# Kernel optimization log

Hardware: AMD Instinct MI355X
Metric: run time of the kernel (lower is better)

The kernel has to match this reference:

```python
import jax, jax.numpy as jnp
import numpy as np

N, D, H, Y = 2048, 768, 12, 64


def setup_inputs() -> dict:
    key = jax.random.key(0)
    kg, kq, kk = jax.random.split(key, 3)
    g = jax.random.normal(kg, (N, D), dtype=jnp.float32)
    Wq = jax.random.normal(kq, (H, Y, D), dtype=jnp.float32)
    Wk = jax.random.normal(kk, (H, Y, D), dtype=jnp.float32)
    return {"g": g, "Wq": Wq, "Wk": Wk}


def reference(g, Wq, Wk):
    # g: [N, D]; Wq, Wk: [H, Y, D]
    beta = 1.0 / jnp.sqrt(jnp.asarray(Y, dtype=g.dtype))
    K = jnp.einsum('kd,hzd->khz', g, Wk)          # [N, H, Y]
    Q = jnp.einsum('qd,hzd->qhz', g, Wq)          # [N, H, Y]
    scores = beta * jnp.einsum('qhz,khz->hqk', Q, K)  # [H, N, N]
    A = jax.nn.logsumexp(scores, axis=-1)         # [H, N]
    return (-1.0 / beta) * A.sum()
```

## Files before the change

kernel.cpp:

```cpp
#include <hip/hip_runtime.h>
#include <hip/hip_bf16.h>

#define NN 2048
#define DD 768
#define HH 12
#define HW 1536
#define SPLITS 4
#define KPW (NN/SPLITS)
#define NCH (KPW/64)
#define LDP 72

typedef __attribute__((ext_vector_type(8))) short bf16x8;
typedef __attribute__((ext_vector_type(4))) float f32x4;

__device__ __forceinline__ float exp2g(float x) { return __builtin_amdgcn_exp2f(x); }
__device__ __forceinline__ float log2g(float x) { return __builtin_amdgcn_logf(x); }

#define QSCALE 0.18033688011112042f

__device__ __forceinline__ short b16(float x) {
  __hip_bfloat16 h = __float2bfloat16(x);
  return *reinterpret_cast<short*>(&h);
}
__device__ __forceinline__ bf16x8 cvt8(float4 a, float4 b, float sc) {
  bf16x8 r;
  r[0] = b16(a.x * sc); r[1] = b16(a.y * sc);
  r[2] = b16(a.z * sc); r[3] = b16(a.w * sc);
  r[4] = b16(b.x * sc); r[5] = b16(b.y * sc);
  r[6] = b16(b.z * sc); r[7] = b16(b.w * sc);
  return r;
}

__global__ __launch_bounds__(256) void proj_kernel(
    const float* __restrict__ g, const float* __restrict__ Wq,
    const float* __restrict__ Wk, __hip_bfloat16* __restrict__ QK,
    float* __restrict__ out) {
  __shared__ __align__(16) __hip_bfloat16 As[2][64 * LDP];
  __shared__ __align__(16) __hip_bfloat16 Bs[2][64 * LDP];
  const int t = threadIdx.x;
  const int wave = t >> 6, lane = t & 63;
  const int lr = lane & 15, lg = lane >> 4;
  const int wm = wave & 1, wn = wave >> 1;
  const int bm = blockIdx.x, bn = blockIdx.y;
  if (bm == 0 && bn == 0 && t == 0) out[0] = 0.0f;

  const float* Wsrc = (bn < 12) ? (Wq + bn * 64 * DD) : (Wk + (bn - 12) * 64 * DD);
  const float sc = (bn < 12) ? QSCALE : 1.0f;

  const int r0 = t >> 3, s0c = (t & 7) * 8;
  const int r1 = r0 + 32;

  f32x4 acc[2][2] = {};

  {
    const float* ga0 = g + (bm * 64 + r0) * DD + s0c;
    const float* ga1 = g + (bm * 64 + r1) * DD + s0c;
    const float* gb0 = Wsrc + r0 * DD + s0c;
    const float* gb1 = Wsrc + r1 * DD + s0c;
    *reinterpret_cast<bf16x8*>(&As[0][r0 * LDP + s0c]) =
        cvt8(*(const float4*)ga0, *(const float4*)(ga0 + 4), 1.0f);
    *reinterpret_cast<bf16x8*>(&As[0][r1 * LDP + s0c]) =
        cvt8(*(const float4*)ga1, *(const float4*)(ga1 + 4), 1.0f);
    *reinterpret_cast<bf16x8*>(&Bs[0][r0 * LDP + s0c]) =
        cvt8(*(const float4*)gb0, *(const float4*)(gb0 + 4), sc);
    *reinterpret_cast<bf16x8*>(&Bs[0][r1 * LDP + s0c]) =
        cvt8(*(const float4*)gb1, *(const float4*)(gb1 + 4), sc);
  }
  __syncthreads();

  for (int it = 0; it < 12; ++it) {
    const int cur = it & 1;
    float4 pa0, pa1, pa2, pa3, pb0, pb1, pb2, pb3;
    if (it < 11) {
      int kt = (it + 1) * 64;
      const float* ga0 = g + (bm * 64 + r0) * DD + kt + s0c;
      const float* ga1 = g + (bm * 64 + r1) * DD + kt + s0c;
      const float* gb0 = Wsrc + r0 * DD + kt + s0c;
      const float* gb1 = Wsrc + r1 * DD + kt + s0c;
      pa0 = *(const float4*)ga0; pa1 = *(const float4*)(ga0 + 4);
      pa2 = *(const float4*)ga1; pa3 = *(const float4*)(ga1 + 4);
      pb0 = *(const float4*)gb0; pb1 = *(const float4*)(gb0 + 4);
      pb2 = *(const float4*)gb1; pb3 = *(const float4*)(gb1 + 4);
    }
#pragma unroll
    for (int ks = 0; ks < 2; ++ks) {
      bf16x8 a[2], b[2];
#pragma unroll
      for (int mt = 0; mt < 2; ++mt)
        a[mt] = *reinterpret_cast<const bf16x8*>(&As[cur][(wm * 32 + mt * 16 + lr) * LDP + ks * 32 + lg * 8]);
#pragma unroll
      for (int nt = 0; nt < 2; ++nt)
        b[nt] = *reinterpret_cast<const bf16x8*>(&Bs[cur][(wn * 32 + nt * 16 + lr) * LDP + ks * 32 + lg * 8]);
#pragma unroll
      for (int mt = 0; mt < 2; ++mt)
#pragma unroll
        for (int nt = 0; nt < 2; ++nt)
          acc[mt][nt] = __builtin_amdgcn_mfma_f32_16x16x32_bf16(a[mt], b[nt], acc[mt][nt], 0, 0, 0);
    }
    if (it < 11) {
      const int nxt = cur ^ 1;
      *reinterpret_cast<bf16x8*>(&As[nxt][r0 * LDP + s0c]) = cvt8(pa0, pa1, 1.0f);
      *reinterpret_cast<bf16x8*>(&As[nxt][r1 * LDP + s0c]) = cvt8(pa2, pa3, 1.0f);
      *reinterpret_cast<bf16x8*>(&Bs[nxt][r0 * LDP + s0c]) = cvt8(pb0, pb1, sc);
      *reinterpret_cast<bf16x8*>(&Bs[nxt][r1 * LDP + s0c]) = cvt8(pb2, pb3, sc);
      __syncthreads();
    }
  }
#pragma unroll
  for (int mt = 0; mt < 2; ++mt) {
    int row = bm * 64 + wm * 32 + mt * 16 + lg * 4;
#pragma unroll
    for (int nt = 0; nt < 2; ++nt) {
      int col = bn * 64 + wn * 32 + nt * 16 + lr;
#pragma unroll
      for (int r = 0; r < 4; ++r)
        QK[(row + r) * HW + col] = __float2bfloat16(acc[mt][nt][r]);
    }
  }
}

__global__ __launch_bounds__(256) void attn_kernel(
    const __hip_bfloat16* __restrict__ QK, float2* __restrict__ part) {
  __shared__ __align__(16) __hip_bfloat16 Ks[2][64 * LDP];
  const int t = threadIdx.x;
  const int wave = t >> 6, lane = t & 63;
  const int lr = lane & 15, lg = lane >> 4;
  const int q0 = blockIdx.x * 128, h = blockIdx.y, sp = blockIdx.z;
  const int k0 = sp * KPW;
  const int r0 = t >> 3, s0 = (t & 7) * 8;
  const int r1 = r0 + 32;
  const int colK = DD + h * 64;

  bf16x8 aq[2][2];
#pragma unroll
  for (int mt = 0; mt < 2; ++mt)
#pragma unroll
    for (int z = 0; z < 2; ++z)
      aq[mt][z] = *reinterpret_cast<const bf16x8*>(
          QK + (q0 + wave * 32 + mt * 16 + lr) * HW + h * 64 + z * 32 + lg * 8);

  *reinterpret_cast<uint4*>(&Ks[0][r0 * LDP + s0]) =
      *reinterpret_cast<const uint4*>(QK + (k0 + r0) * HW + colK + s0);
  *reinterpret_cast<uint4*>(&Ks[0][r1 * LDP + s0]) =
      *reinterpret_cast<const uint4*>(QK + (k0 + r1) * HW + colK + s0);
  __syncthreads();

  float m[2][4], l[2][4];
#pragma unroll
  for (int mt = 0; mt < 2; ++mt)
#pragma unroll
    for (int r = 0; r < 4; ++r) { m[mt][r] = -3.0e38f; l[mt][r] = 0.0f; }

  for (int ci = 0; ci < NCH; ++ci) {
    const int cur = ci & 1;
    uint4 n0, n1;
    if (ci < NCH - 1) {
      int kc = k0 + (ci + 1) * 64;
      n0 = *reinterpret_cast<const uint4*>(QK + (kc + r0) * HW + colK + s0);
      n1 = *reinterpret_cast<const uint4*>(QK + (kc + r1) * HW + colK + s0);
    }
    bf16x8 b[4][2];
#pragma unroll
    for (int nt = 0; nt < 4; ++nt)
#pragma unroll
      for (int z = 0; z < 2; ++z)
        b[nt][z] = *reinterpret_cast<const bf16x8*>(&Ks[cur][(nt * 16 + lr) * LDP + z * 32 + lg * 8]);

    f32x4 s[2][4] = {};
#pragma unroll
    for (int mt = 0; mt < 2; ++mt)
#pragma unroll
      for (int nt = 0; nt < 4; ++nt)
#pragma unroll
        for (int z = 0; z < 2; ++z)
          s[mt][nt] = __builtin_amdgcn_mfma_f32_16x16x32_bf16(aq[mt][z], b[nt][z], s[mt][nt], 0, 0, 0);

#pragma unroll
    for (int mt = 0; mt < 2; ++mt)
#pragma unroll
      for (int r = 0; r < 4; ++r) {
        float v0 = s[mt][0][r], v1 = s[mt][1][r], v2 = s[mt][2][r], v3 = s[mt][3][r];
        float cm = fmaxf(fmaxf(v0, v1), fmaxf(v2, v3));
        float mn = fmaxf(m[mt][r], cm);
        float p = exp2g(v0 - mn) + exp2g(v1 - mn) +
                  exp2g(v2 - mn) + exp2g(v3 - mn);
        l[mt][r] = l[mt][r] * exp2g(m[mt][r] - mn) + p;
        m[mt][r] = mn;
      }
    if (ci < NCH - 1) {
      *reinterpret_cast<uint4*>(&Ks[cur ^ 1][r0 * LDP + s0]) = n0;
      *reinterpret_cast<uint4*>(&Ks[cur ^ 1][r1 * LDP + s0]) = n1;
      __syncthreads();
    }
  }
#pragma unroll
  for (int msk = 1; msk <= 8; msk <<= 1) {
#pragma unroll
    for (int mt = 0; mt < 2; ++mt)
#pragma unroll
      for (int r = 0; r < 4; ++r) {
        float mo = __shfl_xor(m[mt][r], msk);
        float lo = __shfl_xor(l[mt][r], msk);
        float mn = fmaxf(m[mt][r], mo);
        l[mt][r] = l[mt][r] * exp2g(m[mt][r] - mn) + lo * exp2g(mo - mn);
        m[mt][r] = mn;
      }
  }
  if (lr == 0) {
#pragma unroll
    for (int mt = 0; mt < 2; ++mt)
#pragma unroll
      for (int r = 0; r < 4; ++r) {
        int q = q0 + wave * 32 + mt * 16 + lg * 4 + r;
        part[(sp * HH + h) * NN + q] = make_float2(m[mt][r], l[mt][r]);
      }
  }
}

__global__ __launch_bounds__(1024) void reduce_kernel(
    const float2* __restrict__ part, float* __restrict__ out) {
  const int t = threadIdx.x;
  const int row = blockIdx.x * 1024 + t;
  float2 p0 = part[row];
  float2 p1 = part[24576 + row];
  float2 p2 = part[49152 + row];
  float2 p3 = part[73728 + row];
  float mm = fmaxf(fmaxf(p0.x, p1.x), fmaxf(p2.x, p3.x));
  float ll = p0.y * exp2g(p0.x - mm) + p1.y * exp2g(p1.x - mm) +
             p2.y * exp2g(p2.x - mm) + p3.y * exp2g(p3.x - mm);
  float lse = mm + log2g(ll);
#pragma unroll
  for (int msk = 1; msk <= 32; msk <<= 1)
    lse += __shfl_xor(lse, msk);
  __shared__ float wsum[16];
  if ((t & 63) == 0) wsum[t >> 6] = lse;
  __syncthreads();
  if (t == 0) {
    float s = 0.0f;
#pragma unroll
    for (int i = 0; i < 16; ++i) s += wsum[i];
    atomicAdd(out, -5.545177444479562f * s);
  }
}

extern "C" void kernel_launch(void* const* d_in, const int* in_sizes, int n_in,
                              void* d_out, int out_size, void* d_ws, size_t ws_size,
                              hipStream_t stream) {
  const float* g  = (const float*)d_in[0];
  const float* Wq = (const float*)d_in[1];
  const float* Wk = (const float*)d_in[2];
  float* out = (float*)d_out;

  char* ws = (char*)d_ws;
  __hip_bfloat16* QK = (__hip_bfloat16*)ws;
  float2* part = (float2*)(ws + 6291456);

  proj_kernel<<<dim3(32, 24), 256, 0, stream>>>(g, Wq, Wk, QK, out);
  attn_kernel<<<dim3(16, HH, SPLITS), 256, 0, stream>>>(QK, part);
  reduce_kernel<<<24, 1024, 0, stream>>>(part, out);
}
```

Measured before the change: 95.81 us.

## Shrink attention query tile to 64 rows and double key splits to eight

The attention kernel now gives each wave 16 query rows instead of 32, so a block covers 64 queries, and the key dimension is split 8 ways instead of 4. The grid grows from 768 to 3072 blocks, and per-thread register use drops because accumulators and running max/sum state are halved. The reduce kernel is generalized to merge SPLITS partials. The cost is that each K tile loaded into shared memory is reused by half as many query rows, which doubles K traffic and sync overhead per unit of work, and the partial-result buffer doubles in size.

Measured after the change: 97.18 us. No clear change (+1.4%).

```diff
diff --git a/kernel.cpp b/kernel.cpp
--- a/kernel.cpp
+++ b/kernel.cpp
@@ -5,7 +5,7 @@
 #define DD 768
 #define HH 12
 #define HW 1536
-#define SPLITS 4
+#define SPLITS 8
 #define KPW (NN/SPLITS)
 #define NCH (KPW/64)
 #define LDP 72
@@ -125,19 +125,17 @@
   const int t = threadIdx.x;
   const int wave = t >> 6, lane = t & 63;
   const int lr = lane & 15, lg = lane >> 4;
-  const int q0 = blockIdx.x * 128, h = blockIdx.y, sp = blockIdx.z;
+  const int q0 = blockIdx.x * 64, h = blockIdx.y, sp = blockIdx.z;
   const int k0 = sp * KPW;
   const int r0 = t >> 3, s0 = (t & 7) * 8;
   const int r1 = r0 + 32;
   const int colK = DD + h * 64;
 
-  bf16x8 aq[2][2];
-#pragma unroll
-  for (int mt = 0; mt < 2; ++mt)
-#pragma unroll
-    for (int z = 0; z < 2; ++z)
-      aq[mt][z] = *reinterpret_cast<const bf16x8*>(
-          QK + (q0 + wave * 32 + mt * 16 + lr) * HW + h * 64 + z * 32 + lg * 8);
+  bf16x8 aq[2];
+#pragma unroll
+  for (int z = 0; z < 2; ++z)
+    aq[z] = *reinterpret_cast<const bf16x8*>(
+        QK + (q0 + wave * 16 + lr) * HW + h * 64 + z * 32 + lg * 8);
 
   *reinterpret_cast<uint4*>(&Ks[0][r0 * LDP + s0]) =
       *reinterpret_cast<const uint4*>(QK + (k0 + r0) * HW + colK + s0);
@@ -145,11 +143,9 @@
       *reinterpret_cast<const uint4*>(QK + (k0 + r1) * HW + colK + s0);
   __syncthreads();
 
-  float m[2][4], l[2][4];
-#pragma unroll
-  for (int mt = 0; mt < 2; ++mt)
-#pragma unroll
-    for (int r = 0; r < 4; ++r) { m[mt][r] = -3.0e38f; l[mt][r] = 0.0f; }
+  float m[4], l[4];
+#pragma unroll
+  for (int r = 0; r < 4; ++r) { m[r] = -3.0e38f; l[r] = 0.0f; }
 
   for (int ci = 0; ci < NCH; ++ci) {
     const int cur = ci & 1;
@@ -159,34 +155,24 @@
       n0 = *reinterpret_cast<const uint4*>(QK + (kc + r0) * HW + colK + s0);
       n1 = *reinterpret_cast<const uint4*>(QK + (kc + r1) * HW + colK + s0);
     }
-    bf16x8 b[4][2];
+    f32x4 s[4] = {};
 #pragma unroll
     for (int nt = 0; nt < 4; ++nt)
 #pragma unroll
-      for (int z = 0; z < 2; ++z)
-        b[nt][z] = *reinterpret_cast<const bf16x8*>(&Ks[cur][(nt * 16 + lr) * LDP + z * 32 + lg * 8]);
-
-    f32x4 s[2][4] = {};
-#pragma unroll
-    for (int mt = 0; mt < 2; ++mt)
-#pragma unroll
-      for (int nt = 0; nt < 4; ++nt)
-#pragma unroll
-        for (int z = 0; z < 2; ++z)
-          s[mt][nt] = __builtin_amdgcn_mfma_f32_16x16x32_bf16(aq[mt][z], b[nt][z], s[mt][nt], 0, 0, 0);
-
-#pragma unroll
-    for (int mt = 0; mt < 2; ++mt)
-#pragma unroll
-      for (int r = 0; r < 4; ++r) {
-        float v0 = s[mt][0][r], v1 = s[mt][1][r], v2 = s[mt][2][r], v3 = s[mt][3][r];
-        float cm = fmaxf(fmaxf(v0, v1), fmaxf(v2, v3));
-        float mn = fmaxf(m[mt][r], cm);
-        float p = exp2g(v0 - mn) + exp2g(v1 - mn) +
-                  exp2g(v2 - mn) + exp2g(v3 - mn);
-        l[mt][r] = l[mt][r] * exp2g(m[mt][r] - mn) + p;
-        m[mt][r] = mn;
+      for (int z = 0; z < 2; ++z) {
+        bf16x8 b = *reinterpret_cast<const bf16x8*>(&Ks[cur][(nt * 16 + lr) * LDP + z * 32 + lg * 8]);
+        s[nt] = __builtin_amdgcn_mfma_f32_16x16x32_bf16(aq[z], b, s[nt], 0, 0, 0);
       }
+#pragma unroll
+    for (int r = 0; r < 4; ++r) {
+      float v0 = s[0][r], v1 = s[1][r], v2 = s[2][r], v3 = s[3][r];
+      float cm = fmaxf(fmaxf(v0, v1), fmaxf(v2, v3));
+      float mn = fmaxf(m[r], cm);
+      float p = exp2g(v0 - mn) + exp2g(v1 - mn) +
+                exp2g(v2 - mn) + exp2g(v3 - mn);
+      l[r] = l[r] * exp2g(m[r] - mn) + p;
+      m[r] = mn;
+    }
     if (ci < NCH - 1) {
       *reinterpret_cast<uint4*>(&Ks[cur ^ 1][r0 * LDP + s0]) = n0;
       *reinterpret_cast<uint4*>(&Ks[cur ^ 1][r1 * LDP + s0]) = n1;
@@ -196,24 +182,20 @@
 #pragma unroll
   for (int msk = 1; msk <= 8; msk <<= 1) {
 #pragma unroll
-    for (int mt = 0; mt < 2; ++mt)
-#pragma unroll
-      for (int r = 0; r < 4; ++r) {
-        float mo = __shfl_xor(m[mt][r], msk);
-        float lo = __shfl_xor(l[mt][r], msk);
-        float mn = fmaxf(m[mt][r], mo);
-        l[mt][r] = l[mt][r] * exp2g(m[mt][r] - mn) + lo * exp2g(mo - mn);
-        m[mt][r] = mn;
-      }
+    for (int r = 0; r < 4; ++r) {
+      float mo = __shfl_xor(m[r], msk);
+      float lo = __shfl_xor(l[r], msk);
+      float mn = fmaxf(m[r], mo);
+      l[r] = l[r] * exp2g(m[r] - mn) + lo * exp2g(mo - mn);
+      m[r] = mn;
+    }
   }
   if (lr == 0) {
 #pragma unroll
-    for (int mt = 0; mt < 2; ++mt)
-#pragma unroll
-      for (int r = 0; r < 4; ++r) {
-        int q = q0 + wave * 32 + mt * 16 + lg * 4 + r;
-        part[(sp * HH + h) * NN + q] = make_float2(m[mt][r], l[mt][r]);
-      }
+    for (int r = 0; r < 4; ++r) {
+      int q = q0 + wave * 16 + lg * 4 + r;
+      part[(sp * HH + h) * NN + q] = make_float2(m[r], l[r]);
+    }
   }
 }
 
@@ -221,13 +203,16 @@
     const float2* __restrict__ part, float* __restrict__ out) {
   const int t = threadIdx.x;
   const int row = blockIdx.x * 1024 + t;
-  float2 p0 = part[row];
-  float2 p1 = part[24576 + row];
-  float2 p2 = part[49152 + row];
-  float2 p3 = part[73728 + row];
-  float mm = fmaxf(fmaxf(p0.x, p1.x), fmaxf(p2.x, p3.x));
-  float ll = p0.y * exp2g(p0.x - mm) + p1.y * exp2g(p1.x - mm) +
-             p2.y * exp2g(p2.x - mm) + p3.y * exp2g(p3.x - mm);
+  float2 p[SPLITS];
+#pragma unroll
+  for (int sp = 0; sp < SPLITS; ++sp)
+    p[sp] = part[sp * (HH * NN) + row];
+  float mm = -3.0e38f;
+#pragma unroll
+  for (int sp = 0; sp < SPLITS; ++sp) mm = fmaxf(mm, p[sp].x);
+  float ll = 0.0f;
+#pragma unroll
+  for (int sp = 0; sp < SPLITS; ++sp) ll += p[sp].y * exp2g(p[sp].x - mm);
   float lse = mm + log2g(ll);
 #pragma unroll
   for (int msk = 1; msk <= 32; msk <<= 1)
@@ -256,6 +241,6 @@
   float2* part = (float2*)(ws + 6291456);
 
   proj_kernel<<<dim3(32, 24), 256, 0, stream>>>(g, Wq, Wk, QK, out);
-  attn_kernel<<<dim3(16, HH, SPLITS), 256, 0, stream>>>(QK, part);
+  attn_kernel<<<dim3(32, HH, SPLITS), 256, 0, stream>>>(QK, part);
   reduce_kernel<<<24, 1024, 0, stream>>>(part, out);
 }
```
